# Performance work log

Hardware: AMD Instinct MI355X
Metric: run time of the kernel (lower is better)

The kernel has to match this reference:

```python
import jax, jax.numpy as jnp
import numpy as np

N_NODES = 100000
N_EDGES = 1600000
NUM_GRAPHS = 128


def _gcn_layer(x, W, b, senders, receivers, n_node):
    # Linear transform first (cheaper: feature dim small)
    x = x @ W + b  # [N, out]
    ones = jnp.ones(senders.shape[0], dtype=x.dtype)
    deg_s = jax.ops.segment_sum(ones, senders, n_node)     # out-degree
    deg_r = jax.ops.segment_sum(ones, receivers, n_node)   # in-degree
    # symmetric normalization: D^-1/2 A D^-1/2
    x = x * jax.lax.rsqrt(jnp.maximum(deg_s, 1.0))[:, None]
    x = jax.ops.segment_sum(x[senders], receivers, n_node)  # gather-scatter aggregation
    x = x * jax.lax.rsqrt(jnp.maximum(deg_r, 1.0))[:, None]
    return x


def setup_inputs() -> dict:
    key = jax.random.key(0)
    ks = jax.random.split(key, 10)
    x = jax.random.normal(ks[0], (N_NODES, 9), dtype=jnp.float32)
    senders = jax.random.randint(ks[1], (N_EDGES,), 0, N_NODES)
    receivers = jax.random.randint(ks[2], (N_EDGES,), 0, N_NODES)
    batch = jnp.sort(jax.random.randint(ks[3], (N_NODES,), 0, NUM_GRAPHS))
    # learned params (Dense: W [in,out], b [out]) with LeCun-normal-ish scale
    def dense(k, din, dout):
        return jax.random.normal(k, (din, dout), dtype=jnp.float32) / np.sqrt(din)
    W1 = dense(ks[4], 9, 64)
    b1 = jnp.zeros((64,), jnp.float32)
    W2 = dense(ks[5], 64, 128)
    b2 = jnp.zeros((128,), jnp.float32)
    W3 = dense(ks[6], 128, 2)
    b3 = jnp.zeros((2,), jnp.float32)
    return {"x": x, "senders": senders, "receivers": receivers, "batch": batch,
            "num_graphs": NUM_GRAPHS, "W1": W1, "b1": b1, "W2": W2, "b2": b2,
            "W3": W3, "b3": b3}


def reference(x, senders, receivers, batch, num_graphs, W1, b1, W2, b2, W3, b3):
    n_node = x.shape[0]
    x = jax.nn.relu(_gcn_layer(x, W1, b1, senders, receivers, n_node))
    x = jax.nn.relu(_gcn_layer(x, W2, b2, senders, receivers, n_node))
    x = _gcn_layer(x, W3, b3, senders, receivers, n_node)
    # graph-level pooling
    return jax.ops.segment_sum(x, batch, num_graphs)
```

## Files before the change

kernel.cpp:

```cpp
#include <hip/hip_runtime.h>
#include <hip/hip_bf16.h>
#include <cstddef>

#define NBMAX 512
#define BCAP 5120
#define BKCHUNK 3200

typedef unsigned short bf16t;
typedef __attribute__((ext_vector_type(8))) short short8;
typedef __attribute__((ext_vector_type(4))) float f32x4;

static __device__ __forceinline__ float2 up2(unsigned u) {
    return make_float2(__uint_as_float(u << 16), __uint_as_float(u & 0xffff0000u));
}
static __device__ __forceinline__ bf16t f2bf(float f) {
    unsigned u = __float_as_uint(f);
    u += 0x7fffu + ((u >> 16) & 1u);
    return (bf16t)(u >> 16);
}
static __device__ __forceinline__ unsigned pk2(float a, float b) {
    return (unsigned)f2bf(a) | ((unsigned)f2bf(b) << 16);
}

__global__ void k_bucket(const int* __restrict__ S, const int* __restrict__ R,
                         unsigned* __restrict__ bufR, int* __restrict__ degS,
                         int* __restrict__ gCntR,
                         const float* __restrict__ W2, bf16t* __restrict__ W2f,
                         int nE, int nB) {
    __shared__ int histR[NBMAX], lstR[NBMAX], baseR[NBMAX];
    __shared__ int sm[256];
    __shared__ unsigned sortedR[BKCHUNK];
    __shared__ unsigned short bOfR[BKCHUNK];
    int t = threadIdx.x;
    int nSort = gridDim.x - 4;
    if (blockIdx.x >= nSort) {
        int tt = (blockIdx.x - nSort) * blockDim.x + t;
        if (tt < 1024) {
            int nt = tt >> 7, kh = (tt >> 6) & 1, lane = tt & 63;
            int n = nt * 16 + (lane & 15);
            int k0 = kh * 32 + (lane >> 4) * 8;
            uint4 p;
            p.x = pk2(W2[(k0 + 0) * 128 + n], W2[(k0 + 1) * 128 + n]);
            p.y = pk2(W2[(k0 + 2) * 128 + n], W2[(k0 + 3) * 128 + n]);
            p.z = pk2(W2[(k0 + 4) * 128 + n], W2[(k0 + 5) * 128 + n]);
            p.w = pk2(W2[(k0 + 6) * 128 + n], W2[(k0 + 7) * 128 + n]);
            ((uint4*)W2f)[tt] = p;
        }
        return;
    }
    for (int i = t; i < NBMAX; i += 256) histR[i] = 0;
    __syncthreads();
    int chunk = (nE + nSort - 1) / nSort;
    int e0 = blockIdx.x * chunk;
    int e1 = min(e0 + chunk, nE);
    for (int e = e0 + t; e < e1; e += 256) {
        atomicAdd(&histR[R[e] >> 8], 1);
        atomicAdd(&degS[S[e]], 1);
    }
    __syncthreads();
    {
        int c0 = histR[2 * t], c1 = histR[2 * t + 1];
        int ps = c0 + c1;
        sm[t] = ps;
        __syncthreads();
        for (int off = 1; off < 256; off <<= 1) {
            int y = (t >= off) ? sm[t - off] : 0;
            __syncthreads();
            sm[t] += y;
            __syncthreads();
        }
        int ex = sm[t] - ps;
        lstR[2 * t] = ex;
        lstR[2 * t + 1] = ex + c0;
    }
    __syncthreads();
    for (int i = t; i < nB; i += 256) {
        int cR = histR[i];
        baseR[i] = cR ? atomicAdd(&gCntR[i], cR) : 0;
    }
    for (int i = t; i < NBMAX; i += 256) histR[i] = 0;
    __syncthreads();
    for (int e = e0 + t; e < e1; e += 256) {
        int r = R[e], s = S[e];
        int br = r >> 8;
        int p = lstR[br] + atomicAdd(&histR[br], 1);
        sortedR[p] = ((unsigned)(r & 255) << 24) | (unsigned)s;
        bOfR[p] = (unsigned short)br;
    }
    __syncthreads();
    int cnt = e1 - e0;
    for (int i = t; i < cnt; i += 256) {
        int b = bOfR[i];
        int slot = baseR[b] + (i - lstR[b]);
        if (slot < BCAP) bufR[(size_t)b * BCAP + slot] = sortedR[i];
    }
}

__global__ void k_pass2(const unsigned* __restrict__ bufR, const int* __restrict__ gCntR,
                        const int* __restrict__ degS, const float* __restrict__ x,
                        int* __restrict__ csr, int* __restrict__ cur, int* __restrict__ degR,
                        float* __restrict__ inv_r, float* __restrict__ inv_s,
                        bf16t* __restrict__ xs, int nN, int nB) {
    __shared__ int hist[256], incl[256], curs[256];
    __shared__ int sm[256];
    __shared__ int gex[NBMAX];
    int t = threadIdx.x;
    int b = blockIdx.x;
    {
        int c0 = (2 * t < nB) ? gCntR[2 * t] : 0;
        int c1 = (2 * t + 1 < nB) ? gCntR[2 * t + 1] : 0;
        int ps = c0 + c1;
        sm[t] = ps;
        __syncthreads();
        for (int off = 1; off < 256; off <<= 1) {
            int y = (t >= off) ? sm[t - off] : 0;
            __syncthreads();
            sm[t] += y;
            __syncthreads();
        }
        int ex = sm[t] - ps;
        gex[2 * t] = ex;
        gex[2 * t + 1] = ex + c0;
    }
    hist[t] = 0; curs[t] = 0;
    __syncthreads();
    int gb = gex[b];
    int cnt = gCntR[b];
    const unsigned* buf = bufR + (size_t)b * BCAP;
    for (int i = t; i < cnt; i += 256) atomicAdd(&hist[buf[i] >> 24], 1);
    __syncthreads();
    int v = hist[t];
    sm[t] = v;
    __syncthreads();
    for (int off = 1; off < 256; off <<= 1) {
        int y = (t >= off) ? sm[t - off] : 0;
        __syncthreads();
        sm[t] += y;
        __syncthreads();
    }
    incl[t] = sm[t];
    __syncthreads();
    int n0 = b << 8;
    int n = n0 + t;
    if (n < nN) {
        degR[n] = v;
        cur[n] = gb + incl[t];
        inv_r[n] = rsqrtf(fmaxf((float)v, 1.f));
    }
    for (int i = t; i < cnt; i += 256) {
        unsigned p = buf[i];
        int rl = p >> 24;
        int s = p & 0xFFFFFF;
        int pos = gb + (incl[rl] - hist[rl]) + atomicAdd(&curs[rl], 1);
        csr[pos] = s;
    }
    if (n < nN) {
        float is = rsqrtf(fmaxf((float)degS[n], 1.f));
        inv_s[n] = is;
        float w[9];
#pragma unroll
        for (int k = 0; k < 9; k++) w[k] = x[(size_t)n * 9 + k] * is;
        uint4 pa, pb;
        pa.x = pk2(w[0], w[1]); pa.y = pk2(w[2], w[3]);
        pa.z = pk2(w[4], w[5]); pa.w = pk2(w[6], w[7]);
        pb.x = pk2(w[8], is);   pb.y = 0; pb.z = 0; pb.w = 0;
        uint4* o = (uint4*)(xs + (size_t)n * 16);
        o[0] = pa;
        o[1] = pb;
    }
}

__global__ void k_h1f(const unsigned* __restrict__ xs32, const float* __restrict__ W1,
                      const float* __restrict__ b1,
                      const int* __restrict__ csr, const int* __restrict__ cur,
                      const int* __restrict__ degR, const float* __restrict__ inv_r,
                      const float* __restrict__ inv_s,
                      bf16t* __restrict__ h1s, float* __restrict__ warr, int nN) {
    __shared__ float Wl[9 * 64];
    __shared__ float bl[64];
    for (int i = threadIdx.x; i < 9 * 64; i += blockDim.x) Wl[i] = W1[i];
    if (threadIdx.x < 64) bl[threadIdx.x] = b1[threadIdx.x];
    __syncthreads();
    int lane = threadIdx.x & 63;
    int wave = threadIdx.x >> 6;
    int n = blockIdx.x * 16 + wave * 4 + (lane >> 4);
    int nc = min(n, nN - 1);
    int ql = lane & 15;
    int g = ql >> 1;
    int f2 = ql & 1;
    int deg = degR[nc];
    int st = cur[nc] - deg;
    float a0 = 0.f, a1 = 0.f, a2 = 0.f, a3 = 0.f;
    float a4 = 0.f, a5 = 0.f, a6 = 0.f, a7 = 0.f;
    int i = 0;
    for (; i + 16 <= deg; i += 16) {
        int ea = csr[st + i + g];
        int eb = csr[st + i + 8 + g];
        uint4 ua = *(const uint4*)(xs32 + (size_t)ea * 8 + f2 * 4);
        uint4 ub = *(const uint4*)(xs32 + (size_t)eb * 8 + f2 * 4);
        float2 p;
        p = up2(ua.x); a0 += p.x; a1 += p.y;
        p = up2(ua.y); a2 += p.x; a3 += p.y;
        p = up2(ua.z); a4 += p.x; a5 += p.y;
        p = up2(ua.w); a6 += p.x; a7 += p.y;
        p = up2(ub.x); a0 += p.x; a1 += p.y;
        p = up2(ub.y); a2 += p.x; a3 += p.y;
        p = up2(ub.z); a4 += p.x; a5 += p.y;
        p = up2(ub.w); a6 += p.x; a7 += p.y;
    }
    if (i + 8 <= deg) {
        int ea = csr[st + i + g];
        uint4 ua = *(const uint4*)(xs32 + (size_t)ea * 8 + f2 * 4);
        float2 p;
        p = up2(ua.x); a0 += p.x; a1 += p.y;
        p = up2(ua.y); a2 += p.x; a3 += p.y;
        p = up2(ua.z); a4 += p.x; a5 += p.y;
        p = up2(ua.w); a6 += p.x; a7 += p.y;
        i += 8;
    }
    if (g < deg - i) {
        int ea = csr[st + i + g];
        uint4 ua = *(const uint4*)(xs32 + (size_t)ea * 8 + f2 * 4);
        float2 p;
        p = up2(ua.x); a0 += p.x; a1 += p.y;
        p = up2(ua.y); a2 += p.x; a3 += p.y;
        p = up2(ua.z); a4 += p.x; a5 += p.y;
        p = up2(ua.w); a6 += p.x; a7 += p.y;
    }
    a0 += __shfl_xor(a0, 2); a1 += __shfl_xor(a1, 2); a2 += __shfl_xor(a2, 2); a3 += __shfl_xor(a3, 2);
    a4 += __shfl_xor(a4, 2); a5 += __shfl_xor(a5, 2); a6 += __shfl_xor(a6, 2); a7 += __shfl_xor(a7, 2);
    a0 += __shfl_xor(a0, 4); a1 += __shfl_xor(a1, 4); a2 += __shfl_xor(a2, 4); a3 += __shfl_xor(a3, 4);
    a4 += __shfl_xor(a4, 4); a5 += __shfl_xor(a5, 4); a6 += __shfl_xor(a6, 4); a7 += __shfl_xor(a7, 4);
    a0 += __shfl_xor(a0, 8); a1 += __shfl_xor(a1, 8); a2 += __shfl_xor(a2, 8); a3 += __shfl_xor(a3, 8);
    a4 += __shfl_xor(a4, 8); a5 += __shfl_xor(a5, 8); a6 += __shfl_xor(a6, 8); a7 += __shfl_xor(a7, 8);
    int base = lane & 48;
    float xv[9];
    xv[0] = __shfl(a0, base); xv[1] = __shfl(a1, base);
    xv[2] = __shfl(a2, base); xv[3] = __shfl(a3, base);
    xv[4] = __shfl(a4, base); xv[5] = __shfl(a5, base);
    xv[6] = __shfl(a6, base); xv[7] = __shfl(a7, base);
    xv[8] = __shfl(a0, base + 1);
    float w = __shfl(a1, base + 1);
    float ir = inv_r[nc];
    float is = inv_s[nc];
    int c0 = ql * 4;
    float acc[4];
#pragma unroll
    for (int jj = 0; jj < 4; jj++) acc[jj] = w * bl[c0 + jj];
#pragma unroll
    for (int k = 0; k < 9; k++) {
        float4 wv = *(const float4*)(Wl + k * 64 + c0);
        acc[0] += xv[k] * wv.x;
        acc[1] += xv[k] * wv.y;
        acc[2] += xv[k] * wv.z;
        acc[3] += xv[k] * wv.w;
    }
    if (n < nN) {
        float v0 = fmaxf(acc[0] * ir, 0.f) * is;
        float v1 = fmaxf(acc[1] * ir, 0.f) * is;
        float v2 = fmaxf(acc[2] * ir, 0.f) * is;
        float v3 = fmaxf(acc[3] * ir, 0.f) * is;
        uint2 pv;
        pv.x = pk2(v0, v1);
        pv.y = pk2(v2, v3);
        *(uint2*)(h1s + (size_t)n * 64 + c0) = pv;
        if (ql == 0) warr[n] = w;
    }
}

__global__ void __launch_bounds__(128, 8)
k_l2f(const unsigned* __restrict__ h32, const bf16t* __restrict__ W2f,
      const float* __restrict__ b2, const float* __restrict__ W3,
      const float* __restrict__ inv_r, const float* __restrict__ inv_s,
      const float* __restrict__ warr,
      const int* __restrict__ csr, const int* __restrict__ cur,
      const int* __restrict__ degR,
      float* __restrict__ t, float* __restrict__ dout, int outSize, int nN) {
    __shared__ float b2l[128];
    __shared__ float W3l[256];
    __shared__ unsigned zl[16 * 36];
    for (int i = threadIdx.x; i < 128; i += blockDim.x) b2l[i] = b2[i];
    for (int i = threadIdx.x; i < 256; i += blockDim.x) W3l[i] = W3[i];
    if (blockIdx.x == 0)
        for (int i = threadIdx.x; i < outSize; i += blockDim.x) dout[i] = 0.f;
    int lane = threadIdx.x & 63;
    int wave = threadIdx.x >> 6;
    int g3 = lane >> 3;
    int sub = lane & 7;
    int n0b = blockIdx.x * 16;
    {
        int roff = wave * 8 + g3;
        int nc = min(n0b + roff, nN - 1);
        int deg = degR[nc];
        int st = cur[nc] - deg;
        float a0 = 0.f, a1 = 0.f, a2 = 0.f, a3 = 0.f;
        float a4 = 0.f, a5 = 0.f, a6 = 0.f, a7 = 0.f;
        int i = 0;
        for (; i + 4 <= deg; i += 4) {
            int e0 = csr[st + i + 0];
            int e1 = csr[st + i + 1];
            int e2 = csr[st + i + 2];
            int e3 = csr[st + i + 3];
            uint4 u0 = *(const uint4*)(h32 + (size_t)e0 * 32 + sub * 4);
            uint4 u1 = *(const uint4*)(h32 + (size_t)e1 * 32 + sub * 4);
            uint4 u2 = *(const uint4*)(h32 + (size_t)e2 * 32 + sub * 4);
            uint4 u3 = *(const uint4*)(h32 + (size_t)e3 * 32 + sub * 4);
            float2 p;
            p = up2(u0.x); a0 += p.x; a1 += p.y;
            p = up2(u0.y); a2 += p.x; a3 += p.y;
            p = up2(u0.z); a4 += p.x; a5 += p.y;
            p = up2(u0.w); a6 += p.x; a7 += p.y;
            p = up2(u1.x); a0 += p.x; a1 += p.y;
            p = up2(u1.y); a2 += p.x; a3 += p.y;
            p = up2(u1.z); a4 += p.x; a5 += p.y;
            p = up2(u1.w); a6 += p.x; a7 += p.y;
            p = up2(u2.x); a0 += p.x; a1 += p.y;
            p = up2(u2.y); a2 += p.x; a3 += p.y;
            p = up2(u2.z); a4 += p.x; a5 += p.y;
            p = up2(u2.w); a6 += p.x; a7 += p.y;
            p = up2(u3.x); a0 += p.x; a1 += p.y;
            p = up2(u3.y); a2 += p.x; a3 += p.y;
            p = up2(u3.z); a4 += p.x; a5 += p.y;
            p = up2(u3.w); a6 += p.x; a7 += p.y;
        }
        for (; i < deg; i++) {
            int e0 = csr[st + i];
            uint4 u0 = *(const uint4*)(h32 + (size_t)e0 * 32 + sub * 4);
            float2 p;
            p = up2(u0.x); a0 += p.x; a1 += p.y;
            p = up2(u0.y); a2 += p.x; a3 += p.y;
            p = up2(u0.z); a4 += p.x; a5 += p.y;
            p = up2(u0.w); a6 += p.x; a7 += p.y;
        }
        uint4 pv;
        pv.x = pk2(a0, a1);
        pv.y = pk2(a2, a3);
        pv.z = pk2(a4, a5);
        pv.w = pk2(a6, a7);
        *(uint4*)(zl + roff * 36 + sub * 4) = pv;
    }
    __syncthreads();
    int m = lane & 15;
    int q = lane >> 4;
    short8 afr0 = *(const short8*)(zl + m * 36 + q * 4);
    short8 afr1 = *(const short8*)(zl + m * 36 + 16 + q * 4);
    float w4[4], ir4[4], is4[4];
#pragma unroll
    for (int reg = 0; reg < 4; reg++) {
        int nr = min(n0b + q * 4 + reg, nN - 1);
        w4[reg] = warr[nr];
        ir4[reg] = inv_r[nr];
        is4[reg] = inv_s[nr];
    }
    float p0[4] = {0.f, 0.f, 0.f, 0.f}, p1[4] = {0.f, 0.f, 0.f, 0.f};
#pragma unroll
    for (int nt = 0; nt < 8; nt++) {
        short8 b0 = *(const short8*)(W2f + ((size_t)(nt * 2 + 0) * 64 + lane) * 8);
        short8 b1 = *(const short8*)(W2f + ((size_t)(nt * 2 + 1) * 64 + lane) * 8);
        f32x4 acc = {0.f, 0.f, 0.f, 0.f};
        acc = __builtin_amdgcn_mfma_f32_16x16x32_bf16(afr0, b0, acc, 0, 0, 0);
        acc = __builtin_amdgcn_mfma_f32_16x16x32_bf16(afr1, b1, acc, 0, 0, 0);
        int col = nt * 16 + m;
        float bc = b2l[col];
        float w30 = W3l[col * 2 + 0];
        float w31 = W3l[col * 2 + 1];
#pragma unroll
        for (int reg = 0; reg < 4; reg++) {
            float h = fmaxf((acc[reg] + w4[reg] * bc) * ir4[reg], 0.f) * is4[reg];
            p0[reg] += h * w30;
            p1[reg] += h * w31;
        }
    }
#pragma unroll
    for (int mask = 1; mask < 16; mask <<= 1) {
#pragma unroll
        for (int reg = 0; reg < 4; reg++) {
            p0[reg] += __shfl_xor(p0[reg], mask);
            p1[reg] += __shfl_xor(p1[reg], mask);
        }
    }
    if (wave == 0 && m == 0) {
#pragma unroll
        for (int reg = 0; reg < 4; reg++) {
            int nr = n0b + q * 4 + reg;
            if (nr < nN) *(float2*)(t + (size_t)nr * 2) = make_float2(p0[reg], p1[reg]);
        }
    }
}

__global__ void k_poolg(const float* __restrict__ t, const float* __restrict__ inv_r,
                        const float* __restrict__ warr, const float* __restrict__ b3,
                        const int* __restrict__ csr, const int* __restrict__ cur,
                        const int* __restrict__ degR, const int* __restrict__ batch,
                        float* out, int nN, int outSize) {
    __shared__ float sm[256];
    for (int i = threadIdx.x; i < 256; i += blockDim.x) sm[i] = 0.f;
    __syncthreads();
    int tid = blockIdx.x * blockDim.x + threadIdx.x;
    int n = tid >> 3;
    int sub = tid & 7;
    if (n < nN) {
        int deg = degR[n];
        int st = cur[n] - deg;
        float a0 = 0.f, a1 = 0.f, c0 = 0.f, c1 = 0.f;
        int i = sub;
        for (; i + 8 < deg; i += 16) {
            int sa = csr[st + i], sb = csr[st + i + 8];
            float2 va = ((const float2*)t)[sa];
            float2 vb = ((const float2*)t)[sb];
            a0 += va.x; a1 += va.y;
            c0 += vb.x; c1 += vb.y;
        }
        for (; i < deg; i += 8) {
            float2 va = ((const float2*)t)[csr[st + i]];
            a0 += va.x; a1 += va.y;
        }
        float p0 = a0 + c0;
        float p1 = a1 + c1;
        p0 += __shfl_xor(p0, 1); p1 += __shfl_xor(p1, 1);
        p0 += __shfl_xor(p0, 2); p1 += __shfl_xor(p1, 2);
        p0 += __shfl_xor(p0, 4); p1 += __shfl_xor(p1, 4);
        if (sub == 0) {
            float ir = inv_r[n];
            float wb = warr[n] * ir;
            int g = batch[n];
            atomicAdd(&sm[2 * g + 0], p0 * ir + wb * b3[0]);
            atomicAdd(&sm[2 * g + 1], p1 * ir + wb * b3[1]);
        }
    }
    __syncthreads();
    for (int i = threadIdx.x; i < outSize; i += blockDim.x) {
        float v = sm[i];
        if (v != 0.f) atomicAdd(&out[i], v);
    }
}

extern "C" void kernel_launch(void* const* d_in, const int* in_sizes, int n_in,
                              void* d_out, int out_size, void* d_ws, size_t ws_size,
                              hipStream_t stream) {
    const float* x     = (const float*)d_in[0];
    const int*   S     = (const int*)d_in[1];
    const int*   R     = (const int*)d_in[2];
    const int*   batch = (const int*)d_in[3];
    const float* W1 = (const float*)d_in[5];
    const float* b1 = (const float*)d_in[6];
    const float* W2 = (const float*)d_in[7];
    const float* b2 = (const float*)d_in[8];
    const float* W3 = (const float*)d_in[9];
    const float* b3 = (const float*)d_in[10];

    int nN = in_sizes[0] / 9;
    int nE = in_sizes[1];
    int nB = (nN + 255) / 256;

    char* ws = (char*)d_ws;
    int*   cur   = (int*)ws;
    int*   degR  = cur + nN;
    float* inv_s = (float*)(degR + nN);
    float* inv_r = inv_s + nN;
    float* warr  = inv_r + nN;
    int*   degS  = (int*)(warr + nN);
    int*   gCntR = degS + nN;
    int*   csr   = gCntR + NBMAX;
    bf16t* xs    = (bf16t*)(csr + nE);
    bf16t* W2f   = xs + (size_t)nN * 16;
    char*  regA  = (char*)(W2f + 8192);
    unsigned* bufR = (unsigned*)regA;
    bf16t* h1s = (bf16t*)regA;
    float* t   = (float*)(regA + (size_t)NBMAX * BCAP * 5);

    const int B = 256;

    hipMemsetAsync(degS, 0, (size_t)(nN + NBMAX) * 4, stream);
    k_bucket<<<516, B, 0, stream>>>(S, R, bufR, degS, gCntR, W2, W2f, nE, nB);
    k_pass2<<<nB, B, 0, stream>>>(bufR, gCntR, degS, x, csr, cur, degR,
                                  inv_r, inv_s, xs, nN, nB);

    k_h1f<<<(nN + 15) / 16, B, 0, stream>>>((const unsigned*)xs, W1, b1, csr, cur, degR,
                                            inv_r, inv_s, h1s, warr, nN);

    k_l2f<<<(nN + 15) / 16, 128, 0, stream>>>((const unsigned*)h1s, W2f, b2, W3,
                                              inv_r, inv_s, warr, csr, cur, degR,
                                              t, (float*)d_out, out_size, nN);

    k_poolg<<<(nN * 8 + B - 1) / B, B, 0, stream>>>(t, inv_r, warr, b3, csr, cur, degR, batch,
                                                    (float*)d_out, nN, out_size);
}
```

Before: 255.7 us.

## Compute sender degrees via bucketed byte sort instead of global atomics

Replaces the global per-node atomicAdd on degS with a second bucket sort of senders by high bits. Each edge's low byte goes into a per-bucket byte buffer, and k_pass2 builds a shared-memory histogram over those bytes to get out-degrees. The sort grid now scales with the edge count (chunk halved, roughly 1000 blocks) and the large degS memset shrinks to a small counter clear. The aim is to remove 1.6M contended global atomics, paid for with extra LDS atomics, another prefix scan and a byte buffer write and read.

```diff
diff --git a/kernel.cpp b/kernel.cpp
--- a/kernel.cpp
+++ b/kernel.cpp
@@ -4,7 +4,7 @@
 
 #define NBMAX 512
 #define BCAP 5120
-#define BKCHUNK 3200
+#define BKCHUNK 1600
 
 typedef unsigned short bf16t;
 typedef __attribute__((ext_vector_type(8))) short short8;
@@ -23,14 +23,17 @@
 }
 
 __global__ void k_bucket(const int* __restrict__ S, const int* __restrict__ R,
-                         unsigned* __restrict__ bufR, int* __restrict__ degS,
-                         int* __restrict__ gCntR,
+                         unsigned* __restrict__ bufR, unsigned char* __restrict__ bufS,
+                         int* __restrict__ gCntR, int* __restrict__ gCntS,
                          const float* __restrict__ W2, bf16t* __restrict__ W2f,
                          int nE, int nB) {
     __shared__ int histR[NBMAX], lstR[NBMAX], baseR[NBMAX];
+    __shared__ int histS[NBMAX], lstS[NBMAX], baseS[NBMAX];
     __shared__ int sm[256];
     __shared__ unsigned sortedR[BKCHUNK];
     __shared__ unsigned short bOfR[BKCHUNK];
+    __shared__ unsigned char sortedS[BKCHUNK];
+    __shared__ unsigned short bOfS[BKCHUNK];
     int t = threadIdx.x;
     int nSort = gridDim.x - 4;
     if (blockIdx.x >= nSort) {
@@ -48,14 +51,14 @@
         }
         return;
     }
-    for (int i = t; i < NBMAX; i += 256) histR[i] = 0;
+    for (int i = t; i < NBMAX; i += 256) { histR[i] = 0; histS[i] = 0; }
     __syncthreads();
     int chunk = (nE + nSort - 1) / nSort;
     int e0 = blockIdx.x * chunk;
     int e1 = min(e0 + chunk, nE);
     for (int e = e0 + t; e < e1; e += 256) {
         atomicAdd(&histR[R[e] >> 8], 1);
-        atomicAdd(&degS[S[e]], 1);
+        atomicAdd(&histS[S[e] >> 8], 1);
     }
     __syncthreads();
     {
@@ -74,11 +77,29 @@
         lstR[2 * t + 1] = ex + c0;
     }
     __syncthreads();
+    {
+        int c0 = histS[2 * t], c1 = histS[2 * t + 1];
+        int ps = c0 + c1;
+        sm[t] = ps;
+        __syncthreads();
+        for (int off = 1; off < 256; off <<= 1) {
+            int y = (t >= off) ? sm[t - off] : 0;
+            __syncthreads();
+            sm[t] += y;
+            __syncthreads();
+        }
+        int ex = sm[t] - ps;
+        lstS[2 * t] = ex;
+        lstS[2 * t + 1] = ex + c0;
+    }
+    __syncthreads();
     for (int i = t; i < nB; i += 256) {
         int cR = histR[i];
         baseR[i] = cR ? atomicAdd(&gCntR[i], cR) : 0;
-    }
-    for (int i = t; i < NBMAX; i += 256) histR[i] = 0;
+        int cS = histS[i];
+        baseS[i] = cS ? atomicAdd(&gCntS[i], cS) : 0;
+    }
+    for (int i = t; i < NBMAX; i += 256) { histR[i] = 0; histS[i] = 0; }
     __syncthreads();
     for (int e = e0 + t; e < e1; e += 256) {
         int r = R[e], s = S[e];
@@ -86,6 +107,10 @@
         int p = lstR[br] + atomicAdd(&histR[br], 1);
         sortedR[p] = ((unsigned)(r & 255) << 24) | (unsigned)s;
         bOfR[p] = (unsigned short)br;
+        int bs = s >> 8;
+        int p2 = lstS[bs] + atomicAdd(&histS[bs], 1);
+        sortedS[p2] = (unsigned char)(s & 255);
+        bOfS[p2] = (unsigned short)bs;
     }
     __syncthreads();
     int cnt = e1 - e0;
@@ -93,15 +118,19 @@
         int b = bOfR[i];
         int slot = baseR[b] + (i - lstR[b]);
         if (slot < BCAP) bufR[(size_t)b * BCAP + slot] = sortedR[i];
-    }
-}
-
-__global__ void k_pass2(const unsigned* __restrict__ bufR, const int* __restrict__ gCntR,
-                        const int* __restrict__ degS, const float* __restrict__ x,
+        int b2 = bOfS[i];
+        int slot2 = baseS[b2] + (i - lstS[b2]);
+        if (slot2 < BCAP) bufS[(size_t)b2 * BCAP + slot2] = sortedS[i];
+    }
+}
+
+__global__ void k_pass2(const unsigned* __restrict__ bufR, const unsigned char* __restrict__ bufS,
+                        const int* __restrict__ gCntR, const int* __restrict__ gCntS,
+                        const float* __restrict__ x,
                         int* __restrict__ csr, int* __restrict__ cur, int* __restrict__ degR,
                         float* __restrict__ inv_r, float* __restrict__ inv_s,
                         bf16t* __restrict__ xs, int nN, int nB) {
-    __shared__ int hist[256], incl[256], curs[256];
+    __shared__ int hist[256], incl[256], curs[256], histS[256];
     __shared__ int sm[256];
     __shared__ int gex[NBMAX];
     int t = threadIdx.x;
@@ -122,7 +151,7 @@
         gex[2 * t] = ex;
         gex[2 * t + 1] = ex + c0;
     }
-    hist[t] = 0; curs[t] = 0;
+    hist[t] = 0; curs[t] = 0; histS[t] = 0;
     __syncthreads();
     int gb = gex[b];
     int cnt = gCntR[b];
@@ -154,8 +183,12 @@
         int pos = gb + (incl[rl] - hist[rl]) + atomicAdd(&curs[rl], 1);
         csr[pos] = s;
     }
+    int cntS = gCntS[b];
+    const unsigned char* bufs = bufS + (size_t)b * BCAP;
+    for (int i = t; i < cntS; i += 256) atomicAdd(&histS[bufs[i]], 1);
+    __syncthreads();
     if (n < nN) {
-        float is = rsqrtf(fmaxf((float)degS[n], 1.f));
+        float is = rsqrtf(fmaxf((float)histS[t], 1.f));
         inv_s[n] = is;
         float w[9];
 #pragma unroll
@@ -459,21 +492,24 @@
     float* inv_s = (float*)(degR + nN);
     float* inv_r = inv_s + nN;
     float* warr  = inv_r + nN;
-    int*   degS  = (int*)(warr + nN);
-    int*   gCntR = degS + nN;
-    int*   csr   = gCntR + NBMAX;
+    int*   gCntR = (int*)(warr + nN);
+    int*   gCntS = gCntR + NBMAX;
+    int*   csr   = gCntS + NBMAX;
     bf16t* xs    = (bf16t*)(csr + nE);
     bf16t* W2f   = xs + (size_t)nN * 16;
     char*  regA  = (char*)(W2f + 8192);
-    unsigned* bufR = (unsigned*)regA;
+    unsigned*      bufR = (unsigned*)regA;
+    unsigned char* bufS = (unsigned char*)(bufR + (size_t)NBMAX * BCAP);
     bf16t* h1s = (bf16t*)regA;
     float* t   = (float*)(regA + (size_t)NBMAX * BCAP * 5);
 
     const int B = 256;
 
-    hipMemsetAsync(degS, 0, (size_t)(nN + NBMAX) * 4, stream);
-    k_bucket<<<516, B, 0, stream>>>(S, R, bufR, degS, gCntR, W2, W2f, nE, nB);
-    k_pass2<<<nB, B, 0, stream>>>(bufR, gCntR, degS, x, csr, cur, degR,
+    int nSort = (nE + BKCHUNK - 1) / BKCHUNK;
+    if (nSort < 1) nSort = 1;
+    hipMemsetAsync(gCntR, 0, 2 * NBMAX * 4, stream);
+    k_bucket<<<nSort + 4, B, 0, stream>>>(S, R, bufR, bufS, gCntR, gCntS, W2, W2f, nE, nB);
+    k_pass2<<<nB, B, 0, stream>>>(bufR, bufS, gCntR, gCntS, x, csr, cur, degR,
                                   inv_r, inv_s, xs, nN, nB);
 
     k_h1f<<<(nN + 15) / 16, B, 0, stream>>>((const unsigned*)xs, W1, b1, csr, cur, degR,
```

Result: faster. 227.8 us (-10.9%).
